# Kernel tuning notes

Hardware: AMD Instinct MI355X
Metric: run time of the kernel (lower is better)

Reference implementation:

```python
import jax, jax.numpy as jnp
import numpy as np

B, S, H, NH, DH, I, C, P = 4, 1024, 1280, 20, 64, 5120, 13, 8
LN_EPS = 1e-5


def setup_inputs() -> dict:
    key = jax.random.key(0)
    ks = jax.random.split(key, 20)
    n = lambda k, shp, s=0.02: (jax.random.normal(k, shp, jnp.float32) * s)
    return {
        "hidden_states": jax.random.normal(ks[0], (B, S, H), jnp.float32),
        "attention_mask": jnp.ones((B, S), jnp.float32),
        "Wq": n(ks[1], (H, H)), "bq": jnp.zeros((H,), jnp.float32),
        "Wk": n(ks[2], (H, H)), "bk": jnp.zeros((H,), jnp.float32),
        "Wv": n(ks[3], (H, H)), "bv": jnp.zeros((H,), jnp.float32),
        "W_ct1": n(ks[4], (P, C), 0.3), "b_ct1": jnp.zeros((P,), jnp.float32),
        "W_ct2": n(ks[5], (P, C), 0.3), "b_ct2": jnp.zeros((P,), jnp.float32),
        "M": n(ks[6], (C, C), 0.5),
        "bias_scale": jnp.full((1,), 0.5, jnp.float32),
        "W_ptm": n(ks[7], (P, H)), "b_ptm": jnp.zeros((P,), jnp.float32),
        "ln_g": jnp.ones((H,), jnp.float32), "ln_b": jnp.zeros((H,), jnp.float32),
        "Wf1": n(ks[8], (I, H)), "bf1": jnp.zeros((I,), jnp.float32),
        "Wf2": n(ks[9], (H, I)), "bf2": jnp.zeros((H,), jnp.float32),
    }


def reference(hidden_states, attention_mask, Wq, bq, Wk, bk, Wv, bv,
              W_ct1, b_ct1, W_ct2, b_ct2, M, bias_scale, W_ptm, b_ptm,
              ln_g, ln_b, Wf1, bf1, Wf2, bf2):
    h = hidden_states
    # crosstalk bilinear projection: (P,C) @ (C,P) -> (P,P)
    out1 = (M.T @ W_ct1.T + b_ct1).T          # (P, C)
    out2 = M @ W_ct2.T + b_ct2                # (C, P)
    R = out1 @ out2                           # (P, P)
    # ptm_predictor (Linear H->P) + softmax
    ptm = jax.nn.softmax(h @ W_ptm.T + b_ptm, axis=-1)            # (B,S,P)
    Bb = jnp.tanh(jnp.einsum('blc,cd,bmd->blm', ptm, R, ptm)) * bias_scale  # (B,S,S)
    # manual multi-head attention
    q = (h @ Wq.T + bq).reshape(B, S, NH, DH).transpose(0, 2, 1, 3)
    k = (h @ Wk.T + bk).reshape(B, S, NH, DH).transpose(0, 2, 1, 3)
    v = (h @ Wv.T + bv).reshape(B, S, NH, DH).transpose(0, 2, 1, 3)
    scores = jnp.einsum('bhld,bhmd->bhlm', q, k) / np.float32(np.sqrt(DH))
    scores = scores + Bb[:, None]
    scores = scores + (1.0 - attention_mask)[:, None, None, :] * jnp.finfo(h.dtype).min
    probs = jax.nn.softmax(scores, axis=-1)
    ctx = jnp.einsum('bhlm,bhmd->bhld', probs, v)
    ctx = ctx.transpose(0, 2, 1, 3).reshape(B, S, H)
    # residual + LayerNorm
    x = h + ctx
    mu = jnp.mean(x, -1, keepdims=True)
    var = jnp.var(x, -1, keepdims=True)
    x = (x - mu) * jax.lax.rsqrt(var + LN_EPS) * ln_g + ln_b
    # FFN with exact GELU, residual
    ff = jax.nn.gelu(x @ Wf1.T + bf1, approximate=False) @ Wf2.T + bf2
    return x + ff
```

## Files before the change

### kernel.cpp

```cpp
#include <hip/hip_runtime.h>
#include <math.h>

typedef _Float16 f16;
typedef _Float16 f16x2 __attribute__((ext_vector_type(2)));
typedef _Float16 f16x8 __attribute__((ext_vector_type(8)));
typedef _Float16 f16x4 __attribute__((ext_vector_type(4)));
typedef float f32x4 __attribute__((ext_vector_type(4)));

#define B_ 4
#define S_ 1024
#define H_ 1280
#define NH_ 20
#define DH_ 64
#define I_ 5120
#define C_ 13
#define P_ 8
#define LOG2E 1.44269504088896f

__device__ __forceinline__ void store_val(float* p, float v) { *p = v; }
__device__ __forceinline__ void store_val(f16* p, float v) { *p = (f16)v; }

__global__ __launch_bounds__(256) void cvt6_kernel(
    const float* __restrict__ s0, f16* __restrict__ d0, int n0,
    const float* __restrict__ s1, f16* __restrict__ d1, int n1,
    const float* __restrict__ s2, f16* __restrict__ d2, int n2,
    const float* __restrict__ s3, f16* __restrict__ d3, int n3,
    const float* __restrict__ s4, f16* __restrict__ d4, int n4,
    const float* __restrict__ s5, f16* __restrict__ d5, int n5) {
    int seg = blockIdx.y;
    const float* src = (seg == 0) ? s0 : (seg == 1) ? s1 : (seg == 2) ? s2
                     : (seg == 3) ? s3 : (seg == 4) ? s4 : s5;
    f16* dst = (seg == 0) ? d0 : (seg == 1) ? d1 : (seg == 2) ? d2
             : (seg == 3) ? d3 : (seg == 4) ? d4 : d5;
    int n = (seg == 0) ? n0 : (seg == 1) ? n1 : (seg == 2) ? n2
          : (seg == 3) ? n3 : (seg == 4) ? n4 : n5;
    int i = blockIdx.x * 256 + threadIdx.x;
    if (i < n) {
        f32x4 v = ((const f32x4*)src)[i];
        f16x4 o;
#pragma unroll
        for (int e = 0; e < 4; e++) o[e] = (f16)v[e];
        ((f16x4*)dst)[i] = o;
    }
}

__global__ __launch_bounds__(256) void ptm_kernel(const float* __restrict__ hin,
                                                  const float* __restrict__ Wptm,
                                                  const float* __restrict__ bptm,
                                                  const float* __restrict__ Mg,
                                                  const float* __restrict__ W1,
                                                  const float* __restrict__ b1,
                                                  const float* __restrict__ W2,
                                                  const float* __restrict__ b2,
                                                  float* __restrict__ ptm,
                                                  float* __restrict__ tg) {
    __shared__ float o1[P_][C_];
    __shared__ float o2[C_][P_];
    __shared__ float R[P_ * P_];
    int t = threadIdx.x;
    if (t < P_ * C_) {
        int p = t / C_, c = t % C_;
        float s = b1[p];
        for (int k = 0; k < C_; k++) s += Mg[k * C_ + c] * W1[p * C_ + k];
        o1[p][c] = s;
        int c2 = t / P_, p2 = t % P_;
        float s2 = b2[p2];
        for (int k = 0; k < C_; k++) s2 += Mg[c2 * C_ + k] * W2[p2 * C_ + k];
        o2[c2][p2] = s2;
    }
    __syncthreads();
    if (t < P_ * P_) {
        int p = t >> 3, q = t & 7;
        float s = 0.f;
        for (int c = 0; c < C_; c++) s += o1[p][c] * o2[c][q];
        R[t] = s;
    }
    __syncthreads();

    int wv = t >> 6, lane = t & 63;
    int row = blockIdx.x * 4 + wv;
    const float* hrow = hin + (size_t)row * H_;
    float acc[P_] = {};
    for (int i = 0; i < H_ / 64; i++) {
        int k = lane + 64 * i;
        float hv = hrow[k];
#pragma unroll
        for (int p = 0; p < P_; p++) acc[p] += hv * Wptm[p * H_ + k];
    }
#pragma unroll
    for (int p = 0; p < P_; p++) {
#pragma unroll
        for (int o = 32; o >= 1; o >>= 1) acc[p] += __shfl_xor(acc[p], o);
        acc[p] += bptm[p];
    }
    float mx = acc[0];
#pragma unroll
    for (int p = 1; p < P_; p++) mx = fmaxf(mx, acc[p]);
    float sum = 0.f;
#pragma unroll
    for (int p = 0; p < P_; p++) { acc[p] = expf(acc[p] - mx); sum += acc[p]; }
    float rinv = 1.f / sum;
#pragma unroll
    for (int p = 0; p < P_; p++) acc[p] *= rinv;
    float tv[P_];
#pragma unroll
    for (int d = 0; d < P_; d++) {
        float s = 0.f;
#pragma unroll
        for (int c = 0; c < P_; c++) s += acc[c] * R[c * P_ + d];
        tv[d] = s;
    }
    if (lane == 0) {
#pragma unroll
        for (int p = 0; p < P_; p++) {
            ptm[(size_t)row * P_ + p] = acc[p];
            tg[(size_t)row * P_ + p]  = tv[p];
        }
    }
}

__global__ __launch_bounds__(256) void bias_kernel(const float* __restrict__ tg,
                                                   const float* __restrict__ ptm,
                                                   const float* __restrict__ mask,
                                                   const float* __restrict__ bscale_p,
                                                   f16* __restrict__ bb) {
    const int bl = blockIdx.x;
    const int b = bl >> 10;
    const int t = threadIdx.x;
    __shared__ float tl[P_];
    if (t < P_) tl[t] = tg[(size_t)bl * P_ + t];
    __syncthreads();
    const float bscale = bscale_p[0];
    float t0 = tl[0], t1 = tl[1], t2 = tl[2], t3 = tl[3];
    float t4 = tl[4], t5 = tl[5], t6 = tl[6], t7 = tl[7];
#pragma unroll
    for (int i = 0; i < 4; i++) {
        int m = t + 256 * i;
        const float* pm = ptm + ((size_t)b * S_ + m) * P_;
        float4 p0 = *(const float4*)pm;
        float4 p1 = *(const float4*)(pm + 4);
        float d = t0 * p0.x + t1 * p0.y + t2 * p0.z + t3 * p0.w
                + t4 * p1.x + t5 * p1.y + t6 * p1.z + t7 * p1.w;
        float v = (tanhf(d) * bscale + (1.0f - mask[(size_t)b * S_ + m]) * (-30000.0f)) * LOG2E;
        bb[(size_t)bl * S_ + m] = (f16)v;
    }
}

template <int MODE, typename YT>
__device__ __forceinline__ void gemm_body(const f16* __restrict__ X,
                                          const f16* __restrict__ W,
                                          const float* __restrict__ bias,
                                          YT* __restrict__ Y,
                                          const f16* __restrict__ res,
                                          int Ndim, int Kdim, int kbeg, int kend,
                                          int m0, int n0, f16* sA, f16* sB) {
    const int t = threadIdx.x;
    const int lane = t & 63, w = t >> 6;
    const int wr = w >> 1, wc = w & 1;
    const int lr = lane & 15, kq = lane >> 4;

    f32x4 acc[4][4] = {};

    int s_row[4], s_gc[4];
#pragma unroll
    for (int inst = 0; inst < 4; inst++) {
        int ci = t + 256 * inst;
        s_row[inst] = ci >> 3;
        s_gc[inst] = (ci & 7) ^ (s_row[inst] & 7);
    }

    for (int k0 = kbeg; k0 < kend; k0 += 64) {
        __syncthreads();
#pragma unroll
        for (int inst = 0; inst < 4; inst++) {
            int ci = t + 256 * inst;
            __builtin_amdgcn_global_load_lds(
                (const unsigned*)(X + (size_t)(m0 + s_row[inst]) * Kdim + k0 + s_gc[inst] * 8),
                (unsigned*)(sA + ci * 8), 16, 0, 0);
        }
#pragma unroll
        for (int inst = 0; inst < 4; inst++) {
            int ci = t + 256 * inst;
            __builtin_amdgcn_global_load_lds(
                (const unsigned*)(W + (size_t)(n0 + s_row[inst]) * Kdim + k0 + s_gc[inst] * 8),
                (unsigned*)(sB + ci * 8), 16, 0, 0);
        }
        __syncthreads();
#pragma unroll
        for (int ks = 0; ks < 2; ks++) {
            f16x8 af[4], bf[4];
#pragma unroll
            for (int i = 0; i < 4; i++) {
                int row = wr * 64 + i * 16 + lr;
                int cl = (ks * 4 + kq) ^ (row & 7);
                af[i] = *(const f16x8*)(sA + row * 64 + cl * 8);
            }
#pragma unroll
            for (int j = 0; j < 4; j++) {
                int row = wc * 64 + j * 16 + lr;
                int cl = (ks * 4 + kq) ^ (row & 7);
                bf[j] = *(const f16x8*)(sB + row * 64 + cl * 8);
            }
#pragma unroll
            for (int i = 0; i < 4; i++)
#pragma unroll
                for (int j = 0; j < 4; j++)
                    acc[i][j] = __builtin_amdgcn_mfma_f32_16x16x32_f16(af[i], bf[j], acc[i][j], 0, 0, 0);
        }
    }
#pragma unroll
    for (int j = 0; j < 4; j++) {
        int col = n0 + wc * 64 + j * 16 + lr;
        float bcol = (MODE == 3) ? 0.f : bias[col];
#pragma unroll
        for (int i = 0; i < 4; i++) {
#pragma unroll
            for (int rr = 0; rr < 4; rr++) {
                int row = m0 + wr * 64 + i * 16 + kq * 4 + rr;
                float v = acc[i][j][rr] + bcol;
                if (MODE == 1) v = 0.5f * v * (1.0f + erff(v * 0.70710678118654752f));
                if (MODE == 2) v += (float)res[(size_t)row * Ndim + col];
                store_val(&Y[(size_t)row * Ndim + col], v);
            }
        }
    }
}

template <int MODE, typename YT>
__global__ __launch_bounds__(256, 2) void gemm128(const f16* __restrict__ X,
                                                  const f16* __restrict__ W,
                                                  const float* __restrict__ bias,
                                                  YT* __restrict__ Y,
                                                  const f16* __restrict__ res,
                                                  int Ndim, int Kdim) {
    __shared__ f16 sA[128 * 64];
    __shared__ f16 sB[128 * 64];
    gemm_body<MODE, YT>(X, W, bias, Y, res, Ndim, Kdim, 0, Kdim,
                        blockIdx.x * 128, blockIdx.y * 128, sA, sB);
}

__global__ __launch_bounds__(256, 2) void gemm_sk(const f16* __restrict__ X,
                                                  const f16* __restrict__ W,
                                                  float* __restrict__ Pb,
                                                  int Ndim, int Kdim, int Mdim) {
    __shared__ f16 sA[128 * 64];
    __shared__ f16 sB[128 * 64];
    const int kd2 = Kdim >> 1;
    float* Y = Pb + (size_t)blockIdx.z * Mdim * Ndim;
    gemm_body<3, float>(X, W, nullptr, Y, nullptr, Ndim, Kdim,
                        blockIdx.z * kd2, blockIdx.z * kd2 + kd2,
                        blockIdx.x * 128, blockIdx.y * 128, sA, sB);
}

__global__ __launch_bounds__(256) void reduce2_kernel(const float* __restrict__ p0,
                                                      const float* __restrict__ p1,
                                                      const float* __restrict__ bias,
                                                      const f16* __restrict__ res,
                                                      float* __restrict__ out) {
    int i = blockIdx.x * 256 + threadIdx.x;
    int col = (i * 4) % H_;
    f32x4 a = ((const f32x4*)p0)[i];
    f32x4 b = ((const f32x4*)p1)[i];
    f32x4 bc = *(const f32x4*)(bias + col);
    f16x4 r = ((const f16x4*)res)[i];
    f32x4 o;
#pragma unroll
    for (int e = 0; e < 4; e++) o[e] = a[e] + b[e] + bc[e] + (float)r[e];
    ((f32x4*)out)[i] = o;
}

__global__ __launch_bounds__(256, 2) void gemm_qkv(const f16* __restrict__ X,
                                                   const f16* __restrict__ Wq,
                                                   const f16* __restrict__ Wk,
                                                   const f16* __restrict__ Wv,
                                                   const float* __restrict__ bq,
                                                   const float* __restrict__ bk,
                                                   const float* __restrict__ bv,
                                                   f16* __restrict__ qb,
                                                   f16* __restrict__ kb,
                                                   f16* __restrict__ vb) {
    __shared__ f16 sA[128 * 64];
    __shared__ f16 sB[128 * 64];
    const int g = blockIdx.y / 10, nt = blockIdx.y % 10;
    const f16* W = (g == 0) ? Wq : (g == 1) ? Wk : Wv;
    const float* bias = (g == 0) ? bq : (g == 1) ? bk : bv;
    f16* Y = (g == 0) ? qb : (g == 1) ? kb : vb;
    gemm_body<0, f16>(X, W, bias, Y, nullptr, H_, H_, 0, H_,
                      blockIdx.x * 128, nt * 128, sA, sB);
}

__global__ __launch_bounds__(256) void attn_kernel(const f16* __restrict__ q,
                                                   const f16* __restrict__ k,
                                                   const f16* __restrict__ v,
                                                   const f16* __restrict__ bb,
                                                   const float* __restrict__ hin,
                                                   float* __restrict__ xpre) {
    __shared__ f16 sQ[64 * 72];
    __shared__ f16 sK[64 * 72];
    __shared__ f16 sVT[64 * 72];
    __shared__ f16 sP[64 * 72];

    const int t = threadIdx.x;
    const int w = t >> 6, lane = t & 63;
    const int lr = lane & 15, kq = lane >> 4;
    const int l0 = blockIdx.x * 64;
    const int h = blockIdx.y, b = blockIdx.z;
    const size_t base = (size_t)b * S_ * H_ + (size_t)h * DH_;

    for (int idx = t; idx < 512; idx += 256) {
        int r = idx >> 3, c8 = (idx & 7) * 8;
        f16x8 qv = *(const f16x8*)&q[base + (size_t)(l0 + r) * H_ + c8];
#pragma unroll
        for (int e = 0; e < 8; e++) qv[e] = (f16)((float)qv[e] * (0.125f * LOG2E));
        *(f16x8*)&sQ[r * 72 + c8] = qv;
    }
    __syncthreads();
    f16x8 afq[2];
    afq[0] = *(const f16x8*)&sQ[(w * 16 + lr) * 72 + kq * 8];
    afq[1] = *(const f16x8*)&sQ[(w * 16 + lr) * 72 + 32 + kq * 8];

    f32x4 acc_o[4] = {};
    float lstate[4] = {};

    const int vr2 = (t >> 3) * 2, vc8 = (t & 7) * 8;
    const int vmsw = vr2 ^ vc8;

    for (int mt = 0; mt < 16; mt++) {
        const int m0 = mt * 64;
        __syncthreads();
        for (int idx = t; idx < 512; idx += 256) {
            int r = idx >> 3, c8 = (idx & 7) * 8;
            f16x8 kvv = *(const f16x8*)&k[base + (size_t)(m0 + r) * H_ + c8];
            *(f16x8*)&sK[r * 72 + c8] = kvv;
        }
        {
            f16x8 v0 = *(const f16x8*)&v[base + (size_t)(m0 + vr2) * H_ + vc8];
            f16x8 v1 = *(const f16x8*)&v[base + (size_t)(m0 + vr2 + 1) * H_ + vc8];
#pragma unroll
            for (int e = 0; e < 8; e++) {
                f16x2 pk = {v0[e], v1[e]};
                *(f16x2*)&sVT[(vc8 + e) * 72 + vmsw] = pk;
            }
        }
        __syncthreads();

        f32x4 sacc[4] = {};
#pragma unroll
        for (int ks = 0; ks < 2; ks++)
#pragma unroll
            for (int j = 0; j < 4; j++) {
                f16x8 bk = *(const f16x8*)&sK[(j * 16 + lr) * 72 + ks * 32 + kq * 8];
                sacc[j] = __builtin_amdgcn_mfma_f32_16x16x32_f16(afq[ks], bk, sacc[j], 0, 0, 0);
            }
        const f16* bbrow = bb + ((size_t)b * S_ + l0 + w * 16 + kq * 4) * S_ + m0;
#pragma unroll
        for (int j = 0; j < 4; j++)
#pragma unroll
            for (int rr = 0; rr < 4; rr++)
                sacc[j][rr] += (float)bbrow[(size_t)rr * S_ + j * 16 + lr];

#pragma unroll
        for (int j = 0; j < 4; j++)
#pragma unroll
            for (int rr = 0; rr < 4; rr++) {
                float p = __builtin_exp2f(sacc[j][rr]);
                lstate[rr] += p;
                sP[(w * 16 + kq * 4 + rr) * 72 + j * 16 + lr] = (f16)p;
            }
        __syncthreads();

        f16x8 ap[2];
        ap[0] = *(const f16x8*)&sP[(w * 16 + lr) * 72 + kq * 8];
        ap[1] = *(const f16x8*)&sP[(w * 16 + lr) * 72 + 32 + kq * 8];
#pragma unroll
        for (int ks = 0; ks < 2; ks++)
#pragma unroll
            for (int j2 = 0; j2 < 4; j2++) {
                int d = j2 * 16 + lr;
                int s_ = (d >> 3) & 7;
                f16x8 bv = *(const f16x8*)&sVT[d * 72 + 8 * (((ks << 2) + kq) ^ s_)];
                acc_o[j2] = __builtin_amdgcn_mfma_f32_16x16x32_f16(ap[ks], bv, acc_o[j2], 0, 0, 0);
            }
    }

#pragma unroll
    for (int rr = 0; rr < 4; rr++) {
#pragma unroll
        for (int off = 8; off >= 1; off >>= 1) lstate[rr] += __shfl_xor(lstate[rr], off);
    }

#pragma unroll
    for (int rr = 0; rr < 4; rr++) {
        float linv = 1.0f / lstate[rr];
        int tok = l0 + w * 16 + kq * 4 + rr;
        size_t obase = base + (size_t)tok * H_;
#pragma unroll
        for (int j2 = 0; j2 < 4; j2++) {
            int d = j2 * 16 + lr;
            xpre[obase + d] = hin[obase + d] + acc_o[j2][rr] * linv;
        }
    }
}

__global__ __launch_bounds__(256) void ln_kernel(const float* __restrict__ xpre,
                                                 const float* __restrict__ g,
                                                 const float* __restrict__ bb,
                                                 f16* __restrict__ xln) {
    int row = blockIdx.x, t = threadIdx.x;
    const float* xr = xpre + (size_t)row * H_;
    float xv[5], s1 = 0.f, s2 = 0.f;
#pragma unroll
    for (int i = 0; i < 5; i++) {
        float v = xr[t + 256 * i];
        xv[i] = v; s1 += v; s2 += v * v;
    }
#pragma unroll
    for (int o = 32; o >= 1; o >>= 1) { s1 += __shfl_xor(s1, o); s2 += __shfl_xor(s2, o); }
    __shared__ float r1[4], r2[4];
    int wv = t >> 6, lane = t & 63;
    if (lane == 0) { r1[wv] = s1; r2[wv] = s2; }
    __syncthreads();
    float m1 = (r1[0] + r1[1] + r1[2] + r1[3]) * (1.0f / H_);
    float m2 = (r2[0] + r2[1] + r2[2] + r2[3]) * (1.0f / H_);
    float rstd = rsqrtf(m2 - m1 * m1 + 1e-5f);
#pragma unroll
    for (int i = 0; i < 5; i++) {
        int c = t + 256 * i;
        float v = (xv[i] - m1) * rstd * g[c] + bb[c];
        xln[(size_t)row * H_ + c] = (f16)v;
    }
}

extern "C" void kernel_launch(void* const* d_in, const int* in_sizes, int n_in,
                              void* d_out, int out_size, void* d_ws, size_t ws_size,
                              hipStream_t stream) {
    (void)in_sizes; (void)n_in; (void)out_size; (void)ws_size;
    const float* hin  = (const float*)d_in[0];
    const float* mask = (const float*)d_in[1];
    const float* Wq = (const float*)d_in[2];  const float* bq = (const float*)d_in[3];
    const float* Wk = (const float*)d_in[4];  const float* bk = (const float*)d_in[5];
    const float* Wv = (const float*)d_in[6];  const float* bv = (const float*)d_in[7];
    const float* Wct1 = (const float*)d_in[8];  const float* bct1 = (const float*)d_in[9];
    const float* Wct2 = (const float*)d_in[10]; const float* bct2 = (const float*)d_in[11];
    const float* Mg = (const float*)d_in[12];   const float* bscale = (const float*)d_in[13];
    const float* Wptm = (const float*)d_in[14]; const float* bptm = (const float*)d_in[15];
    const float* lng = (const float*)d_in[16];  const float* lnb = (const float*)d_in[17];
    const float* Wf1 = (const float*)d_in[18];  const float* bf1 = (const float*)d_in[19];
    const float* Wf2 = (const float*)d_in[20];  const float* bf2 = (const float*)d_in[21];

    char* ws = (char*)d_ws;
    const size_t SZ_PT  = (size_t)B_ * S_ * P_ * 4;
    const size_t SZ_H16 = (size_t)B_ * S_ * H_ * 2;
    const size_t SZ_H32 = (size_t)B_ * S_ * H_ * 4;
    const size_t SZ_WH  = (size_t)H_ * H_ * 2;
    const size_t SZ_WI  = (size_t)I_ * H_ * 2;
    float* ptm  = (float*)(ws + 256);
    float* tg   = (float*)(ws + 256 + SZ_PT);
    char* A0    = ws + 256 + 2 * SZ_PT;
    f16* hin16  = (f16*)(A0);
    f16* qb     = (f16*)(A0 + SZ_H16);
    f16* kb     = (f16*)(A0 + 2 * SZ_H16);
    f16* vb     = (f16*)(A0 + 3 * SZ_H16);
    float* xpre = (float*)(A0 + 4 * SZ_H16);
    f16* xln    = (f16*)(A0 + 4 * SZ_H16 + SZ_H32);
    f16* bbias  = (f16*)(A0 + 5 * SZ_H16 + SZ_H32);
    char* WA    = A0 + 5 * SZ_H16 + SZ_H32 + (size_t)B_ * S_ * S_ * 2;
    f16* Wq16   = (f16*)(WA);
    f16* Wk16   = (f16*)(WA + SZ_WH);
    f16* Wv16   = (f16*)(WA + 2 * SZ_WH);
    f16* Wf116  = (f16*)(WA + 3 * SZ_WH);
    f16* Wf216  = (f16*)(WA + 3 * SZ_WH + SZ_WI);
    f16* g1     = (f16*)(A0);
    float* pbuf = (float*)(WA + 3 * SZ_WH + 2 * SZ_WI);

    const int NH4 = (B_ * S_ * H_) / 4, NW4 = (H_ * H_) / 4, NI4 = (I_ * H_) / 4;
    cvt6_kernel<<<dim3((NI4 + 255) / 256, 6), 256, 0, stream>>>(
        hin, hin16, NH4, Wq, Wq16, NW4, Wk, Wk16, NW4,
        Wv, Wv16, NW4, Wf1, Wf116, NI4, Wf2, Wf216, NI4);

    ptm_kernel<<<S_ * B_ / 4, 256, 0, stream>>>(hin, Wptm, bptm,
                                                Mg, Wct1, bct1, Wct2, bct2, ptm, tg);
    bias_kernel<<<B_ * S_, 256, 0, stream>>>(tg, ptm, mask, bscale, bbias);
    gemm_qkv<<<dim3(32, 30), 256, 0, stream>>>(hin16, Wq16, Wk16, Wv16, bq, bk, bv, qb, kb, vb);
    attn_kernel<<<dim3(S_ / 64, NH_, B_), 256, 0, stream>>>(qb, kb, vb, bbias, hin, xpre);
    ln_kernel<<<B_ * S_, 256, 0, stream>>>(xpre, lng, lnb, xln);
    gemm128<1, f16><<<dim3(32, I_ / 128), 256, 0, stream>>>(xln, Wf116, bf1, g1, nullptr, I_, H_);
    gemm_sk<<<dim3(32, 10, 2), 256, 0, stream>>>(g1, Wf216, pbuf, H_, I_, B_ * S_);
    reduce2_kernel<<<(B_ * S_ * H_) / 4 / 256, 256, 0, stream>>>(
        pbuf, pbuf + (size_t)B_ * S_ * H_, bf2, xln, (float*)d_out);
}
```

Before: 465.7 us.

## Use tanh-form GELU, exp-based tanh, fp16 split-K partials, staged bias tile

Replaces the exact erf GELU in the FFN1 epilogue with a tanh-approximation computed through exp2, and the tanhf in the pair-bias kernel with an exp2-based formula. The split-K FFN2 partial sums are now stored in fp16 instead of fp32, halving the partial-buffer traffic read back by the reduce kernel. The attention kernel stages each 64x64 tile of the additive bias into shared memory with vectorized loads instead of scattered per-lane global reads. These trade accuracy (tanh-GELU in place of the exact erf form, fp16 rounding of partial sums) for cheaper math and less memory traffic.

```diff
diff --git a/kernel.cpp b/kernel.cpp
--- a/kernel.cpp
+++ b/kernel.cpp
@@ -19,6 +19,13 @@
 
 __device__ __forceinline__ void store_val(float* p, float v) { *p = v; }
 __device__ __forceinline__ void store_val(f16* p, float v) { *p = (f16)v; }
+
+__device__ __forceinline__ float fast_gelu(float v) {
+    float u = v * (0.7978845608f + v * v * 0.0356774081f);
+    u = fminf(fmaxf(u, -20.f), 20.f);
+    float e = __builtin_exp2f(u * 2.88539008178f);
+    return v * e / (e + 1.0f);
+}
 
 __global__ __launch_bounds__(256) void cvt6_kernel(
     const float* __restrict__ s0, f16* __restrict__ d0, int n0,
@@ -141,7 +148,10 @@
         float4 p1 = *(const float4*)(pm + 4);
         float d = t0 * p0.x + t1 * p0.y + t2 * p0.z + t3 * p0.w
                 + t4 * p1.x + t5 * p1.y + t6 * p1.z + t7 * p1.w;
-        float v = (tanhf(d) * bscale + (1.0f - mask[(size_t)b * S_ + m]) * (-30000.0f)) * LOG2E;
+        d = fminf(fmaxf(d, -20.f), 20.f);
+        float e = __builtin_exp2f(d * 2.88539008178f);
+        float th = (e - 1.0f) / (e + 1.0f);
+        float v = (th * bscale + (1.0f - mask[(size_t)b * S_ + m]) * (-30000.0f)) * LOG2E;
         bb[(size_t)bl * S_ + m] = (f16)v;
     }
 }
@@ -218,7 +228,7 @@
             for (int rr = 0; rr < 4; rr++) {
                 int row = m0 + wr * 64 + i * 16 + kq * 4 + rr;
                 float v = acc[i][j][rr] + bcol;
-                if (MODE == 1) v = 0.5f * v * (1.0f + erff(v * 0.70710678118654752f));
+                if (MODE == 1) v = fast_gelu(v);
                 if (MODE == 2) v += (float)res[(size_t)row * Ndim + col];
                 store_val(&Y[(size_t)row * Ndim + col], v);
             }
@@ -241,31 +251,31 @@
 
 __global__ __launch_bounds__(256, 2) void gemm_sk(const f16* __restrict__ X,
                                                   const f16* __restrict__ W,
-                                                  float* __restrict__ Pb,
+                                                  f16* __restrict__ Pb,
                                                   int Ndim, int Kdim, int Mdim) {
     __shared__ f16 sA[128 * 64];
     __shared__ f16 sB[128 * 64];
     const int kd2 = Kdim >> 1;
-    float* Y = Pb + (size_t)blockIdx.z * Mdim * Ndim;
-    gemm_body<3, float>(X, W, nullptr, Y, nullptr, Ndim, Kdim,
-                        blockIdx.z * kd2, blockIdx.z * kd2 + kd2,
-                        blockIdx.x * 128, blockIdx.y * 128, sA, sB);
-}
-
-__global__ __launch_bounds__(256) void reduce2_kernel(const float* __restrict__ p0,
-                                                      const float* __restrict__ p1,
+    f16* Y = Pb + (size_t)blockIdx.z * Mdim * Ndim;
+    gemm_body<3, f16>(X, W, nullptr, Y, nullptr, Ndim, Kdim,
+                      blockIdx.z * kd2, blockIdx.z * kd2 + kd2,
+                      blockIdx.x * 128, blockIdx.y * 128, sA, sB);
+}
+
+__global__ __launch_bounds__(256) void reduce2_kernel(const f16* __restrict__ p0,
+                                                      const f16* __restrict__ p1,
                                                       const float* __restrict__ bias,
                                                       const f16* __restrict__ res,
                                                       float* __restrict__ out) {
     int i = blockIdx.x * 256 + threadIdx.x;
     int col = (i * 4) % H_;
-    f32x4 a = ((const f32x4*)p0)[i];
-    f32x4 b = ((const f32x4*)p1)[i];
+    f16x4 a = ((const f16x4*)p0)[i];
+    f16x4 b = ((const f16x4*)p1)[i];
     f32x4 bc = *(const f32x4*)(bias + col);
     f16x4 r = ((const f16x4*)res)[i];
     f32x4 o;
 #pragma unroll
-    for (int e = 0; e < 4; e++) o[e] = a[e] + b[e] + bc[e] + (float)r[e];
+    for (int e = 0; e < 4; e++) o[e] = (float)a[e] + (float)b[e] + bc[e] + (float)r[e];
     ((f32x4*)out)[i] = o;
 }
 
@@ -299,6 +309,7 @@
     __shared__ f16 sK[64 * 72];
     __shared__ f16 sVT[64 * 72];
     __shared__ f16 sP[64 * 72];
+    __shared__ f16 sBB[64 * 72];
 
     const int t = threadIdx.x;
     const int w = t >> 6, lane = t & 63;
@@ -332,6 +343,8 @@
             int r = idx >> 3, c8 = (idx & 7) * 8;
             f16x8 kvv = *(const f16x8*)&k[base + (size_t)(m0 + r) * H_ + c8];
             *(f16x8*)&sK[r * 72 + c8] = kvv;
+            *(f16x8*)&sBB[r * 72 + c8] =
+                *(const f16x8*)&bb[((size_t)b * S_ + l0 + r) * S_ + m0 + c8];
         }
         {
             f16x8 v0 = *(const f16x8*)&v[base + (size_t)(m0 + vr2) * H_ + vc8];
@@ -352,12 +365,11 @@
                 f16x8 bk = *(const f16x8*)&sK[(j * 16 + lr) * 72 + ks * 32 + kq * 8];
                 sacc[j] = __builtin_amdgcn_mfma_f32_16x16x32_f16(afq[ks], bk, sacc[j], 0, 0, 0);
             }
-        const f16* bbrow = bb + ((size_t)b * S_ + l0 + w * 16 + kq * 4) * S_ + m0;
 #pragma unroll
         for (int j = 0; j < 4; j++)
 #pragma unroll
             for (int rr = 0; rr < 4; rr++)
-                sacc[j][rr] += (float)bbrow[(size_t)rr * S_ + j * 16 + lr];
+                sacc[j][rr] += (float)sBB[(w * 16 + kq * 4 + rr) * 72 + j * 16 + lr];
 
 #pragma unroll
         for (int j = 0; j < 4; j++)
@@ -471,7 +483,7 @@
     f16* Wf116  = (f16*)(WA + 3 * SZ_WH);
     f16* Wf216  = (f16*)(WA + 3 * SZ_WH + SZ_WI);
     f16* g1     = (f16*)(A0);
-    float* pbuf = (float*)(WA + 3 * SZ_WH + 2 * SZ_WI);
+    f16* pbuf   = (f16*)(WA + 3 * SZ_WH + 2 * SZ_WI);
 
     const int NH4 = (B_ * S_ * H_) / 4, NW4 = (H_ * H_) / 4, NI4 = (I_ * H_) / 4;
     cvt6_kernel<<<dim3((NI4 + 255) / 256, 6), 256, 0, stream>>>(
```

Result: no change. 467.1 us (+0.3%).
